# Performance work log

Measured on AMD Instinct MI355X. Metric: run time of the kernel, lower is better.

## Reference

```python
import jax, jax.numpy as jnp
import numpy as np

N_NODES = 100000
N_EDGES = 1600000
D_IN = 128
D_OUT = 128


def setup_inputs() -> dict:
    key = jax.random.key(0)
    k_x, k_r, k_c, k_v, k_w = jax.random.split(key, 5)
    X = jax.random.normal(k_x, (N_NODES, D_IN), dtype=jnp.float32)
    A_rows = jax.random.randint(k_r, (N_EDGES,), 0, N_NODES, dtype=jnp.int32)
    A_cols = jax.random.randint(k_c, (N_EDGES,), 0, N_NODES, dtype=jnp.int32)
    A_vals = jax.random.uniform(k_v, (N_EDGES,), dtype=jnp.float32)
    # Xavier-uniform linear weight [out, in], zero bias (matches reset_parameters)
    limit = float(np.sqrt(6.0 / (D_IN + D_OUT)))
    W = jax.random.uniform(k_w, (D_OUT, D_IN), dtype=jnp.float32, minval=-limit, maxval=limit)
    b = jnp.zeros((D_OUT,), dtype=jnp.float32)
    return {"X": X, "A_rows": A_rows, "A_cols": A_cols, "A_vals": A_vals, "W": W, "b": b}


def reference(X, A_rows, A_cols, A_vals, W, b):
    # h = A_sparse @ X  (COO SpMM: gather neighbor features, scale, scatter-add by row)
    msgs = A_vals[:, None] * X[A_cols]          # [E, D_IN]
    h = jax.ops.segment_sum(msgs, A_rows, num_segments=N_NODES)  # [N, D_IN]
    # dense linear projection
    return h @ W.T + b
```

## Files before the change

### kernel.cpp

```cpp
#include <hip/hip_runtime.h>

#define N_NODES_C 100000
#define N_EDGES_C 1600000
#define D_C 128
#define NBKT 1563
#define RPB 64
#define CAP 1536
#define CAP_H 768
#define PTILE 4096
#define NPB ((N_EDGES_C + PTILE - 1) / PTILE)
#define NGB ((N_NODES_C + 63) / 64)
#define WB_STRIDE 136

static __device__ __forceinline__ unsigned short f2bf(float x) {
    unsigned u = __float_as_uint(x);
    unsigned r = 0x7fffu + ((u >> 16) & 1u);
    return (unsigned short)((u + r) >> 16);
}
static __device__ __forceinline__ float bflo(unsigned u) { return __uint_as_float(u << 16); }
static __device__ __forceinline__ float bfhi(unsigned u) { return __uint_as_float(u & 0xffff0000u); }

typedef __attribute__((ext_vector_type(8))) __bf16 bf16x8;
typedef __attribute__((ext_vector_type(4))) float f32x4;
union FragU { uint4 u; bf16x8 b; };

__global__ __launch_bounds__(256) void prep(const float* __restrict__ W,
                                            unsigned short* __restrict__ Wbf,
                                            int* __restrict__ gcount) {
    int t = blockIdx.x * 256 + threadIdx.x;
    if (t < 4096) {
        float4 w = ((const float4*)W)[t];
        uint2 p;
        p.x = (unsigned)f2bf(w.x) | ((unsigned)f2bf(w.y) << 16);
        p.y = (unsigned)f2bf(w.z) | ((unsigned)f2bf(w.w) << 16);
        ((uint2*)Wbf)[t] = p;
    } else {
        int j = t - 4096;
        if (j < NBKT) gcount[j] = 0;
    }
}

union SMemF {
    struct {
        int lhist[NBKT];
        int lbase[NBKT];
        unsigned short ebkt[PTILE];
        unsigned short ernk[PTILE];
    } part;
    unsigned short ytile[4][16 * WB_STRIDE];
};

__global__ __launch_bounds__(256) void fused(const float* __restrict__ X,
                                             const int* __restrict__ rows,
                                             const int* __restrict__ cols,
                                             const float* __restrict__ vals,
                                             const unsigned short* __restrict__ Wbf,
                                             int* __restrict__ gcount,
                                             int2* __restrict__ staging,
                                             unsigned short* __restrict__ Y,
                                             int n, int E) {
    __shared__ SMemF sm;
    const int tid = threadIdx.x;

    if (blockIdx.x < NPB) {
        const int t0 = blockIdx.x * PTILE;

        for (int i = tid; i < NBKT; i += 256) sm.part.lhist[i] = 0;
        __syncthreads();

#pragma unroll
        for (int k = 0; k < PTILE / 256; ++k) {
            int e = t0 + k * 256 + tid;
            if (e < E) {
                int bkt = rows[e] >> 6;
                int rnk = atomicAdd(&sm.part.lhist[bkt], 1);
                sm.part.ebkt[k * 256 + tid] = (unsigned short)bkt;
                sm.part.ernk[k * 256 + tid] = (unsigned short)rnk;
            }
        }
        __syncthreads();

        for (int i = tid; i < NBKT; i += 256)
            sm.part.lbase[i] = sm.part.lhist[i] ? atomicAdd(&gcount[i], sm.part.lhist[i]) : 0;
        __syncthreads();

#pragma unroll
        for (int k = 0; k < PTILE / 256; ++k) {
            int e = t0 + k * 256 + tid;
            if (e < E) {
                int li = k * 256 + tid;
                int bkt = sm.part.ebkt[li];
                int dst = sm.part.lbase[bkt] + sm.part.ernk[li];
                if (dst < CAP) {
                    int rl = rows[e] & (RPB - 1);
                    int2 p;
                    p.x = cols[e] | (rl << 17);
                    p.y = __float_as_int(vals[e]);
                    staging[(long)bkt * CAP + dst] = p;
                }
            }
        }
        return;
    }

    const int g = blockIdx.x - NPB;
    const int wave = tid >> 6;
    const int lane = tid & 63;
    const int m16 = lane & 15;
    const int quad = lane >> 4;

    const int row0 = g * 64 + wave * 16;
    int row = row0 + m16;
    int rowc = (row < n) ? row : (n - 1);

    FragU a[4];
    const float* xp = X + (long)rowc * D_C + quad * 8;
#pragma unroll
    for (int s = 0; s < 4; ++s) {
        float4 x0 = *(const float4*)(xp + s * 32);
        float4 x1 = *(const float4*)(xp + s * 32 + 4);
        a[s].u.x = (unsigned)f2bf(x0.x) | ((unsigned)f2bf(x0.y) << 16);
        a[s].u.y = (unsigned)f2bf(x0.z) | ((unsigned)f2bf(x0.w) << 16);
        a[s].u.z = (unsigned)f2bf(x1.x) | ((unsigned)f2bf(x1.y) << 16);
        a[s].u.w = (unsigned)f2bf(x1.z) | ((unsigned)f2bf(x1.w) << 16);
    }

    f32x4 acc[8];
#pragma unroll
    for (int t = 0; t < 8; ++t) acc[t] = (f32x4){0.f, 0.f, 0.f, 0.f};

#pragma unroll
    for (int s = 0; s < 4; ++s) {
#pragma unroll
        for (int t = 0; t < 8; ++t) {
            FragU bf;
            bf.u = *(const uint4*)&Wbf[(t * 16 + m16) * D_C + s * 32 + quad * 8];
            acc[t] = __builtin_amdgcn_mfma_f32_16x16x32_bf16(a[s].b, bf.b, acc[t], 0, 0, 0);
        }
    }

    unsigned short* yt = sm.ytile[wave];
#pragma unroll
    for (int t = 0; t < 8; ++t)
#pragma unroll
        for (int r = 0; r < 4; ++r)
            yt[(quad * 4 + r) * WB_STRIDE + t * 16 + m16] = f2bf(acc[t][r]);
    __syncthreads();

#pragma unroll
    for (int h = 0; h < 2; ++h) {
        int row_l = h * 8 + (lane >> 3);
        int orow = row0 + row_l;
        if (orow < n) {
            const unsigned short* src = &yt[row_l * WB_STRIDE + (lane & 7) * 16];
            uint4 v0 = *(const uint4*)(src);
            uint4 v1 = *(const uint4*)(src + 8);
            uint4* dst = (uint4*)&Y[(long)orow * D_C + (lane & 7) * 16];
            dst[0] = v0;
            dst[1] = v1;
        }
    }
}

__global__ __launch_bounds__(256) void sort_aggregate(const int* __restrict__ gcount,
                                                      const int2* __restrict__ staging,
                                                      const unsigned short* __restrict__ Y,
                                                      const float* __restrict__ bias,
                                                      float* __restrict__ out, int n) {
    __shared__ int2 pl[CAP_H];
    __shared__ int hist[32];
    __shared__ int lcur[32];
    __shared__ int rbegL[32];
    __shared__ int rcntL[32];

    const int bb = blockIdx.x >> 1;
    const int half = blockIdx.x & 1;
    const int tid = threadIdx.x;
    int cnt = gcount[bb];
    if (cnt > CAP) cnt = CAP;
    const long s = (long)bb * CAP;

    if (tid < 32) hist[tid] = 0;
    __syncthreads();

    const unsigned* sx = (const unsigned*)(staging + s);
    for (int i = tid; i < cnt; i += 256) {
        int rl = sx[2 * i] >> 17;
        if ((rl >> 5) == half) atomicAdd(&hist[rl & 31], 1);
    }
    __syncthreads();

    int v = (tid < 32) ? hist[tid] : 0;
    for (int off = 1; off < 32; off <<= 1) {
        int t = (tid >= off && tid < 32) ? hist[tid - off] : 0;
        __syncthreads();
        if (tid < 32) hist[tid] += t;
        __syncthreads();
    }
    if (tid < 32) {
        int excl = hist[tid] - v;
        lcur[tid] = excl;
        rbegL[tid] = excl;
        rcntL[tid] = v;
    }
    __syncthreads();

    for (int i = tid; i < cnt; i += 256) {
        int2 p = staging[s + i];
        int rl = ((unsigned)p.x) >> 17;
        if ((rl >> 5) == half) {
            int slot = atomicAdd(&lcur[rl & 31], 1);
            if (slot < CAP_H) pl[slot] = p;
        }
    }
    __syncthreads();

    const int lane = tid & 15;
    const unsigned short* Yl = Y + lane * 8;
    float4 b0 = *(const float4*)&bias[lane * 8];
    float4 b1 = *(const float4*)&bias[lane * 8 + 4];

#pragma unroll
    for (int pass = 0; pass < 2; ++pass) {
        int rlocal = pass * 16 + (tid >> 4);
        int row = bb * RPB + half * 32 + rlocal;
        if (row >= n) continue;

        int i = rbegL[rlocal];
        int e = i + rcntL[rlocal];
        if (e > CAP_H) e = CAP_H;

        float acc[8];
        acc[0] = b0.x; acc[1] = b0.y; acc[2] = b0.z; acc[3] = b0.w;
        acc[4] = b1.x; acc[5] = b1.y; acc[6] = b1.z; acc[7] = b1.w;

        for (; i + 8 <= e; i += 8) {
            int2 p[8];
            uint4 y[8];
#pragma unroll
            for (int u = 0; u < 8; ++u) p[u] = pl[i + u];
#pragma unroll
            for (int u = 0; u < 8; ++u)
                y[u] = *(const uint4*)&Yl[(long)(p[u].x & 0x1FFFF) * D_C];
#pragma unroll
            for (int u = 0; u < 8; ++u) {
                float v2 = __int_as_float(p[u].y);
                acc[0] += v2 * bflo(y[u].x); acc[1] += v2 * bfhi(y[u].x);
                acc[2] += v2 * bflo(y[u].y); acc[3] += v2 * bfhi(y[u].y);
                acc[4] += v2 * bflo(y[u].z); acc[5] += v2 * bfhi(y[u].z);
                acc[6] += v2 * bflo(y[u].w); acc[7] += v2 * bfhi(y[u].w);
            }
        }
        for (; i + 4 <= e; i += 4) {
            int2 p[4];
            uint4 y[4];
#pragma unroll
            for (int u = 0; u < 4; ++u) p[u] = pl[i + u];
#pragma unroll
            for (int u = 0; u < 4; ++u)
                y[u] = *(const uint4*)&Yl[(long)(p[u].x & 0x1FFFF) * D_C];
#pragma unroll
            for (int u = 0; u < 4; ++u) {
                float v2 = __int_as_float(p[u].y);
                acc[0] += v2 * bflo(y[u].x); acc[1] += v2 * bfhi(y[u].x);
                acc[2] += v2 * bflo(y[u].y); acc[3] += v2 * bfhi(y[u].y);
                acc[4] += v2 * bflo(y[u].z); acc[5] += v2 * bfhi(y[u].z);
                acc[6] += v2 * bflo(y[u].w); acc[7] += v2 * bfhi(y[u].w);
            }
        }
        for (; i < e; ++i) {
            int2 p = pl[i];
            uint4 y = *(const uint4*)&Yl[(long)(p.x & 0x1FFFF) * D_C];
            float v2 = __int_as_float(p.y);
            acc[0] += v2 * bflo(y.x); acc[1] += v2 * bfhi(y.x);
            acc[2] += v2 * bflo(y.y); acc[3] += v2 * bfhi(y.y);
            acc[4] += v2 * bflo(y.z); acc[5] += v2 * bfhi(y.z);
            acc[6] += v2 * bflo(y.w); acc[7] += v2 * bfhi(y.w);
        }

        f32x4 o0 = {acc[0], acc[1], acc[2], acc[3]};
        f32x4 o1 = {acc[4], acc[5], acc[6], acc[7]};
        f32x4* op = (f32x4*)&out[(long)row * D_C + lane * 8];
        __builtin_nontemporal_store(o0, op);
        __builtin_nontemporal_store(o1, op + 1);
    }
}

__global__ __launch_bounds__(256) void gemm_mfma(const float* __restrict__ X,
                                                 const float* __restrict__ W,
                                                 unsigned short* __restrict__ Y, int n) {
    __shared__ unsigned short Wb[128 * WB_STRIDE];

    const int tid = threadIdx.x;
    const int wave = tid >> 6;
    const int lane = tid & 63;
    const int m16 = lane & 15;
    const int quad = lane >> 4;

    const int row0 = blockIdx.x * 64 + wave * 16;
    int row = row0 + m16;
    int rowc = (row < n) ? row : (n - 1);

    float4 xv[4][2];
    const float* xp = X + (long)rowc * D_C + quad * 8;
#pragma unroll
    for (int s = 0; s < 4; ++s) {
        xv[s][0] = *(const float4*)(xp + s * 32);
        xv[s][1] = *(const float4*)(xp + s * 32 + 4);
    }

    for (int i = tid; i < 128 * 32; i += 256) {
        int o = i >> 5;
        int k4 = (i & 31) * 4;
        float4 w = *(const float4*)&W[o * 128 + k4];
        uint2 p;
        p.x = (unsigned)f2bf(w.x) | ((unsigned)f2bf(w.y) << 16);
        p.y = (unsigned)f2bf(w.z) | ((unsigned)f2bf(w.w) << 16);
        *(uint2*)&Wb[o * WB_STRIDE + k4] = p;
    }
    __syncthreads();

    FragU a[4];
#pragma unroll
    for (int s = 0; s < 4; ++s) {
        a[s].u.x = (unsigned)f2bf(xv[s][0].x) | ((unsigned)f2bf(xv[s][0].y) << 16);
        a[s].u.y = (unsigned)f2bf(xv[s][0].z) | ((unsigned)f2bf(xv[s][0].w) << 16);
        a[s].u.z = (unsigned)f2bf(xv[s][1].x) | ((unsigned)f2bf(xv[s][1].y) << 16);
        a[s].u.w = (unsigned)f2bf(xv[s][1].z) | ((unsigned)f2bf(xv[s][1].w) << 16);
    }

    f32x4 acc[8];
#pragma unroll
    for (int t = 0; t < 8; ++t) acc[t] = (f32x4){0.f, 0.f, 0.f, 0.f};

#pragma unroll
    for (int s = 0; s < 4; ++s) {
#pragma unroll
        for (int t = 0; t < 8; ++t) {
            FragU bf;
            bf.u = *(const uint4*)&Wb[(t * 16 + m16) * WB_STRIDE + s * 32 + quad * 8];
            acc[t] = __builtin_amdgcn_mfma_f32_16x16x32_bf16(a[s].b, bf.b, acc[t], 0, 0, 0);
        }
    }

#pragma unroll
    for (int t = 0; t < 8; ++t) {
#pragma unroll
        for (int r = 0; r < 4; ++r) {
            int orow = row0 + quad * 4 + r;
            if (orow < n) Y[(long)orow * D_C + t * 16 + m16] = f2bf(acc[t][r]);
        }
    }
}

__global__ __launch_bounds__(256) void init_out(const float* __restrict__ b,
                                                float* __restrict__ out, int n) {
    int idx = blockIdx.x * 256 + threadIdx.x;
    int total = n * (D_C / 4);
    if (idx < total) {
        int o4 = idx & (D_C / 4 - 1);
        ((float4*)out)[idx] = ((const float4*)b)[o4];
    }
}

__global__ __launch_bounds__(256) void scatter_edges(const int* __restrict__ rows,
                                                     const int* __restrict__ cols,
                                                     const float* __restrict__ vals,
                                                     const unsigned short* __restrict__ Y,
                                                     float* __restrict__ out, int E) {
    int e = blockIdx.x * 8 + (threadIdx.x >> 5);
    if (e >= E) return;
    int lane = threadIdx.x & 31;
    int row = rows[e];
    int col = cols[e];
    float v = vals[e];
    uint2 y = *(const uint2*)&Y[(long)col * D_C + lane * 4];
    float* dst = out + (long)row * D_C + lane * 4;
    unsafeAtomicAdd(dst + 0, v * bflo(y.x));
    unsafeAtomicAdd(dst + 1, v * bfhi(y.x));
    unsafeAtomicAdd(dst + 2, v * bflo(y.y));
    unsafeAtomicAdd(dst + 3, v * bfhi(y.y));
}

extern "C" void kernel_launch(void* const* d_in, const int* in_sizes, int n_in,
                              void* d_out, int out_size, void* d_ws, size_t ws_size,
                              hipStream_t stream) {
    const float* X  = (const float*)d_in[0];
    const int*   Ar = (const int*)d_in[1];
    const int*   Ac = (const int*)d_in[2];
    const float* Av = (const float*)d_in[3];
    const float* W  = (const float*)d_in[4];
    const float* b  = (const float*)d_in[5];
    float* out = (float*)d_out;

    unsigned short* Y = (unsigned short*)d_ws;
    int2* staging = (int2*)(Y + 12800000);
    unsigned short* Wbf = (unsigned short*)(staging + (size_t)NBKT * CAP);
    int* gcount = (int*)(Wbf + 16384);
    size_t need = (size_t)12800000 * 2 + (size_t)NBKT * CAP * 8 + 32768 + (size_t)NBKT * 4;

    if (ws_size >= need) {
        prep<<<23, 256, 0, stream>>>(W, Wbf, gcount);
        fused<<<NPB + NGB, 256, 0, stream>>>(X, Ar, Ac, Av, Wbf, gcount, staging, Y,
                                             N_NODES_C, N_EDGES_C);
        sort_aggregate<<<2 * NBKT, 256, 0, stream>>>(gcount, staging, Y, b, out, N_NODES_C);
    } else {
        gemm_mfma<<<(N_NODES_C + 63) / 64, 256, 0, stream>>>(X, W, Y, N_NODES_C);
        init_out<<<(N_NODES_C * (D_C / 4) + 255) / 256, 256, 0, stream>>>(b, out, N_NODES_C);
        scatter_edges<<<(N_EDGES_C + 7) / 8, 256, 0, stream>>>(Ar, Ac, Av, Y, out, N_EDGES_C);
    }
}
```

Baseline: 242.0 us.

## Merge prep, partition/GEMM and aggregate into one cooperative persistent kernel

After: 412.4 us. 70.4% more time.

```diff
diff --git a/kernel.cpp b/kernel.cpp
--- a/kernel.cpp
+++ b/kernel.cpp
@@ -1,4 +1,7 @@
 #include <hip/hip_runtime.h>
+#include <hip/hip_cooperative_groups.h>
+
+namespace cg = cooperative_groups;
 
 #define N_NODES_C 100000
 #define N_EDGES_C 1600000
@@ -7,7 +10,7 @@
 #define RPB 64
 #define CAP 1536
 #define CAP_H 768
-#define PTILE 4096
+#define PTILE 2048
 #define NPB ((N_EDGES_C + PTILE - 1) / PTILE)
 #define NGB ((N_NODES_C + 63) / 64)
 #define WB_STRIDE 136
@@ -23,6 +26,292 @@
 typedef __attribute__((ext_vector_type(8))) __bf16 bf16x8;
 typedef __attribute__((ext_vector_type(4))) float f32x4;
 union FragU { uint4 u; bf16x8 b; };
+
+union SMemAll {
+    struct {
+        int lhist[NBKT];
+        int lbase[NBKT];
+        unsigned short ebkt[PTILE];
+        unsigned short ernk[PTILE];
+    } part;
+    unsigned short ytile[4][16 * WB_STRIDE];
+    struct {
+        int2 pl[CAP_H];
+        int hist[32];
+        int lcur[32];
+        int rb[32];
+        int rc[32];
+    } agg;
+};
+
+static __device__ __forceinline__ void partition_item(SMemAll& sm, int item,
+        const int* __restrict__ rows, const int* __restrict__ cols,
+        const float* __restrict__ vals, int* __restrict__ gcount,
+        int2* __restrict__ staging, int E) {
+    const int tid = threadIdx.x;
+    const int t0 = item * PTILE;
+
+    for (int i = tid; i < NBKT; i += 256) sm.part.lhist[i] = 0;
+    __syncthreads();
+
+#pragma unroll
+    for (int k = 0; k < PTILE / 256; ++k) {
+        int e = t0 + k * 256 + tid;
+        if (e < E) {
+            int bkt = rows[e] >> 6;
+            int rnk = atomicAdd(&sm.part.lhist[bkt], 1);
+            sm.part.ebkt[k * 256 + tid] = (unsigned short)bkt;
+            sm.part.ernk[k * 256 + tid] = (unsigned short)rnk;
+        }
+    }
+    __syncthreads();
+
+    for (int i = tid; i < NBKT; i += 256)
+        sm.part.lbase[i] = sm.part.lhist[i] ? atomicAdd(&gcount[i], sm.part.lhist[i]) : 0;
+    __syncthreads();
+
+#pragma unroll
+    for (int k = 0; k < PTILE / 256; ++k) {
+        int e = t0 + k * 256 + tid;
+        if (e < E) {
+            int li = k * 256 + tid;
+            int bkt = sm.part.ebkt[li];
+            int dst = sm.part.lbase[bkt] + sm.part.ernk[li];
+            if (dst < CAP) {
+                int rl = rows[e] & (RPB - 1);
+                int2 p;
+                p.x = cols[e] | (rl << 17);
+                p.y = __float_as_int(vals[e]);
+                staging[(long)bkt * CAP + dst] = p;
+            }
+        }
+    }
+}
+
+static __device__ __forceinline__ void gemm_item(SMemAll& sm, int g,
+        const float* __restrict__ X, const unsigned short* __restrict__ Wbf,
+        unsigned short* __restrict__ Y, int n) {
+    const int tid = threadIdx.x;
+    const int wave = tid >> 6;
+    const int lane = tid & 63;
+    const int m16 = lane & 15;
+    const int quad = lane >> 4;
+
+    const int row0 = g * 64 + wave * 16;
+    int row = row0 + m16;
+    int rowc = (row < n) ? row : (n - 1);
+
+    FragU a[4];
+    const float* xp = X + (long)rowc * D_C + quad * 8;
+#pragma unroll
+    for (int s = 0; s < 4; ++s) {
+        float4 x0 = *(const float4*)(xp + s * 32);
+        float4 x1 = *(const float4*)(xp + s * 32 + 4);
+        a[s].u.x = (unsigned)f2bf(x0.x) | ((unsigned)f2bf(x0.y) << 16);
+        a[s].u.y = (unsigned)f2bf(x0.z) | ((unsigned)f2bf(x0.w) << 16);
+        a[s].u.z = (unsigned)f2bf(x1.x) | ((unsigned)f2bf(x1.y) << 16);
+        a[s].u.w = (unsigned)f2bf(x1.z) | ((unsigned)f2bf(x1.w) << 16);
+    }
+
+    f32x4 acc[8];
+#pragma unroll
+    for (int t = 0; t < 8; ++t) acc[t] = (f32x4){0.f, 0.f, 0.f, 0.f};
+
+#pragma unroll
+    for (int s = 0; s < 4; ++s) {
+#pragma unroll
+        for (int t = 0; t < 8; ++t) {
+            FragU bf;
+            bf.u = *(const uint4*)&Wbf[(t * 16 + m16) * D_C + s * 32 + quad * 8];
+            acc[t] = __builtin_amdgcn_mfma_f32_16x16x32_bf16(a[s].b, bf.b, acc[t], 0, 0, 0);
+        }
+    }
+
+    unsigned short* yt = sm.ytile[wave];
+#pragma unroll
+    for (int t = 0; t < 8; ++t)
+#pragma unroll
+        for (int r = 0; r < 4; ++r)
+            yt[(quad * 4 + r) * WB_STRIDE + t * 16 + m16] = f2bf(acc[t][r]);
+    __syncthreads();
+
+#pragma unroll
+    for (int h = 0; h < 2; ++h) {
+        int row_l = h * 8 + (lane >> 3);
+        int orow = row0 + row_l;
+        if (orow < n) {
+            const unsigned short* src = &yt[row_l * WB_STRIDE + (lane & 7) * 16];
+            uint4 v0 = *(const uint4*)(src);
+            uint4 v1 = *(const uint4*)(src + 8);
+            uint4* dst = (uint4*)&Y[(long)orow * D_C + (lane & 7) * 16];
+            dst[0] = v0;
+            dst[1] = v1;
+        }
+    }
+}
+
+static __device__ __forceinline__ void agg_item(SMemAll& sm, int item,
+        const int* __restrict__ gcount, const int2* __restrict__ staging,
+        const unsigned short* __restrict__ Y, const float* __restrict__ bias,
+        float* __restrict__ out, int n) {
+    const int bb = item >> 1;
+    const int half = item & 1;
+    const int tid = threadIdx.x;
+    int cnt = gcount[bb];
+    if (cnt > CAP) cnt = CAP;
+    const long s = (long)bb * CAP;
+
+    if (tid < 32) sm.agg.hist[tid] = 0;
+    __syncthreads();
+
+    const unsigned* sx = (const unsigned*)(staging + s);
+    for (int i = tid; i < cnt; i += 256) {
+        int rl = sx[2 * i] >> 17;
+        if ((rl >> 5) == half) atomicAdd(&sm.agg.hist[rl & 31], 1);
+    }
+    __syncthreads();
+
+    int v = (tid < 32) ? sm.agg.hist[tid] : 0;
+    for (int off = 1; off < 32; off <<= 1) {
+        int t = (tid >= off && tid < 32) ? sm.agg.hist[tid - off] : 0;
+        __syncthreads();
+        if (tid < 32) sm.agg.hist[tid] += t;
+        __syncthreads();
+    }
+    if (tid < 32) {
+        int excl = sm.agg.hist[tid] - v;
+        sm.agg.lcur[tid] = excl;
+        sm.agg.rb[tid] = excl;
+        sm.agg.rc[tid] = v;
+    }
+    __syncthreads();
+
+    for (int i = tid; i < cnt; i += 256) {
+        int2 p = staging[s + i];
+        int rl = ((unsigned)p.x) >> 17;
+        if ((rl >> 5) == half) {
+            int slot = atomicAdd(&sm.agg.lcur[rl & 31], 1);
+            if (slot < CAP_H) sm.agg.pl[slot] = p;
+        }
+    }
+    __syncthreads();
+
+    const int lane = tid & 15;
+    const unsigned short* Yl = Y + lane * 8;
+    float4 b0 = *(const float4*)&bias[lane * 8];
+    float4 b1 = *(const float4*)&bias[lane * 8 + 4];
+
+#pragma unroll
+    for (int pass = 0; pass < 2; ++pass) {
+        int rlocal = pass * 16 + (tid >> 4);
+        int row = bb * RPB + half * 32 + rlocal;
+        if (row >= n) continue;
+
+        int i = sm.agg.rb[rlocal];
+        int e = i + sm.agg.rc[rlocal];
+        if (e > CAP_H) e = CAP_H;
+
+        float acc[8];
+        acc[0] = b0.x; acc[1] = b0.y; acc[2] = b0.z; acc[3] = b0.w;
+        acc[4] = b1.x; acc[5] = b1.y; acc[6] = b1.z; acc[7] = b1.w;
+
+        for (; i + 8 <= e; i += 8) {
+            int2 p[8];
+            uint4 y[8];
+#pragma unroll
+            for (int u = 0; u < 8; ++u) p[u] = sm.agg.pl[i + u];
+#pragma unroll
+            for (int u = 0; u < 8; ++u)
+                y[u] = *(const uint4*)&Yl[(long)(p[u].x & 0x1FFFF) * D_C];
+#pragma unroll
+            for (int u = 0; u < 8; ++u) {
+                float v2 = __int_as_float(p[u].y);
+                acc[0] += v2 * bflo(y[u].x); acc[1] += v2 * bfhi(y[u].x);
+                acc[2] += v2 * bflo(y[u].y); acc[3] += v2 * bfhi(y[u].y);
+                acc[4] += v2 * bflo(y[u].z); acc[5] += v2 * bfhi(y[u].z);
+                acc[6] += v2 * bflo(y[u].w); acc[7] += v2 * bfhi(y[u].w);
+            }
+        }
+        for (; i + 4 <= e; i += 4) {
+            int2 p[4];
+            uint4 y[4];
+#pragma unroll
+            for (int u = 0; u < 4; ++u) p[u] = sm.agg.pl[i + u];
+#pragma unroll
+            for (int u = 0; u < 4; ++u)
+                y[u] = *(const uint4*)&Yl[(long)(p[u].x & 0x1FFFF) * D_C];
+#pragma unroll
+            for (int u = 0; u < 4; ++u) {
+                float v2 = __int_as_float(p[u].y);
+                acc[0] += v2 * bflo(y[u].x); acc[1] += v2 * bfhi(y[u].x);
+                acc[2] += v2 * bflo(y[u].y); acc[3] += v2 * bfhi(y[u].y);
+                acc[4] += v2 * bflo(y[u].z); acc[5] += v2 * bfhi(y[u].z);
+                acc[6] += v2 * bflo(y[u].w); acc[7] += v2 * bfhi(y[u].w);
+            }
+        }
+        for (; i < e; ++i) {
+            int2 p = sm.agg.pl[i];
+            uint4 y = *(const uint4*)&Yl[(long)(p.x & 0x1FFFF) * D_C];
+            float v2 = __int_as_float(p.y);
+            acc[0] += v2 * bflo(y.x); acc[1] += v2 * bfhi(y.x);
+            acc[2] += v2 * bflo(y.y); acc[3] += v2 * bfhi(y.y);
+            acc[4] += v2 * bflo(y.z); acc[5] += v2 * bfhi(y.z);
+            acc[6] += v2 * bflo(y.w); acc[7] += v2 * bfhi(y.w);
+        }
+
+        f32x4 o0 = {acc[0], acc[1], acc[2], acc[3]};
+        f32x4 o1 = {acc[4], acc[5], acc[6], acc[7]};
+        f32x4* op = (f32x4*)&out[(long)row * D_C + lane * 8];
+        __builtin_nontemporal_store(o0, op);
+        __builtin_nontemporal_store(o1, op + 1);
+    }
+}
+
+__global__ __launch_bounds__(256) void fused_all(const float* __restrict__ X,
+                                                 const int* __restrict__ rows,
+                                                 const int* __restrict__ cols,
+                                                 const float* __restrict__ vals,
+                                                 const float* __restrict__ W,
+                                                 const float* __restrict__ bias,
+                                                 unsigned short* __restrict__ Wbf,
+                                                 int* __restrict__ gcount,
+                                                 int2* __restrict__ staging,
+                                                 unsigned short* __restrict__ Y,
+                                                 float* __restrict__ out,
+                                                 int n, int E) {
+    __shared__ SMemAll sm;
+    cg::grid_group grid = cg::this_grid();
+    const int nb = gridDim.x;
+
+    for (int t = blockIdx.x * 256 + threadIdx.x; t < 4096 + NBKT; t += nb * 256) {
+        if (t < 4096) {
+            float4 w = ((const float4*)W)[t];
+            uint2 p;
+            p.x = (unsigned)f2bf(w.x) | ((unsigned)f2bf(w.y) << 16);
+            p.y = (unsigned)f2bf(w.z) | ((unsigned)f2bf(w.w) << 16);
+            ((uint2*)Wbf)[t] = p;
+        } else {
+            gcount[t - 4096] = 0;
+        }
+    }
+    __threadfence();
+    grid.sync();
+
+    for (int item = blockIdx.x; item < NPB + NGB; item += nb) {
+        __syncthreads();
+        if (item < NPB)
+            partition_item(sm, item, rows, cols, vals, gcount, staging, E);
+        else
+            gemm_item(sm, item - NPB, X, Wbf, Y, n);
+    }
+    __threadfence();
+    grid.sync();
+
+    for (int item = blockIdx.x; item < 2 * NBKT; item += nb) {
+        __syncthreads();
+        agg_item(sm, item, gcount, staging, Y, bias, out, n);
+    }
+}
 
 __global__ __launch_bounds__(256) void prep(const float* __restrict__ W,
                                             unsigned short* __restrict__ Wbf,
@@ -40,16 +329,6 @@
     }
 }
 
-union SMemF {
-    struct {
-        int lhist[NBKT];
-        int lbase[NBKT];
-        unsigned short ebkt[PTILE];
-        unsigned short ernk[PTILE];
-    } part;
-    unsigned short ytile[4][16 * WB_STRIDE];
-};
-
 __global__ __launch_bounds__(256) void fused(const float* __restrict__ X,
                                              const int* __restrict__ rows,
                                              const int* __restrict__ cols,
@@ -59,107 +338,11 @@
                                              int2* __restrict__ staging,
                                              unsigned short* __restrict__ Y,
                                              int n, int E) {
-    __shared__ SMemF sm;
-    const int tid = threadIdx.x;
-
-    if (blockIdx.x < NPB) {
-        const int t0 = blockIdx.x * PTILE;
-
-        for (int i = tid; i < NBKT; i += 256) sm.part.lhist[i] = 0;
-        __syncthreads();
-
-#pragma unroll
-        for (int k = 0; k < PTILE / 256; ++k) {
-            int e = t0 + k * 256 + tid;
-            if (e < E) {
-                int bkt = rows[e] >> 6;
-                int rnk = atomicAdd(&sm.part.lhist[bkt], 1);
-                sm.part.ebkt[k * 256 + tid] = (unsigned short)bkt;
-                sm.part.ernk[k * 256 + tid] = (unsigned short)rnk;
-            }
-        }
-        __syncthreads();
-
-        for (int i = tid; i < NBKT; i += 256)
-            sm.part.lbase[i] = sm.part.lhist[i] ? atomicAdd(&gcount[i], sm.part.lhist[i]) : 0;
-        __syncthreads();
-
-#pragma unroll
-        for (int k = 0; k < PTILE / 256; ++k) {
-            int e = t0 + k * 256 + tid;
-            if (e < E) {
-                int li = k * 256 + tid;
-                int bkt = sm.part.ebkt[li];
-                int dst = sm.part.lbase[bkt] + sm.part.ernk[li];
-                if (dst < CAP) {
-                    int rl = rows[e] & (RPB - 1);
-                    int2 p;
-                    p.x = cols[e] | (rl << 17);
-                    p.y = __float_as_int(vals[e]);
-                    staging[(long)bkt * CAP + dst] = p;
-                }
-            }
-        }
-        return;
-    }
-
-    const int g = blockIdx.x - NPB;
-    const int wave = tid >> 6;
-    const int lane = tid & 63;
-    const int m16 = lane & 15;
-    const int quad = lane >> 4;
-
-    const int row0 = g * 64 + wave * 16;
-    int row = row0 + m16;
-    int rowc = (row < n) ? row : (n - 1);
-
-    FragU a[4];
-    const float* xp = X + (long)rowc * D_C + quad * 8;
-#pragma unroll
-    for (int s = 0; s < 4; ++s) {
-        float4 x0 = *(const float4*)(xp + s * 32);
-        float4 x1 = *(const float4*)(xp + s * 32 + 4);
-        a[s].u.x = (unsigned)f2bf(x0.x) | ((unsigned)f2bf(x0.y) << 16);
-        a[s].u.y = (unsigned)f2bf(x0.z) | ((unsigned)f2bf(x0.w) << 16);
-        a[s].u.z = (unsigned)f2bf(x1.x) | ((unsigned)f2bf(x1.y) << 16);
-        a[s].u.w = (unsigned)f2bf(x1.z) | ((unsigned)f2bf(x1.w) << 16);
-    }
-
-    f32x4 acc[8];
-#pragma unroll
-    for (int t = 0; t < 8; ++t) acc[t] = (f32x4){0.f, 0.f, 0.f, 0.f};
-
-#pragma unroll
-    for (int s = 0; s < 4; ++s) {
-#pragma unroll
-        for (int t = 0; t < 8; ++t) {
-            FragU bf;
-            bf.u = *(const uint4*)&Wbf[(t * 16 + m16) * D_C + s * 32 + quad * 8];
-            acc[t] = __builtin_amdgcn_mfma_f32_16x16x32_bf16(a[s].b, bf.b, acc[t], 0, 0, 0);
-        }
-    }
-
-    unsigned short* yt = sm.ytile[wave];
-#pragma unroll
-    for (int t = 0; t < 8; ++t)
-#pragma unroll
-        for (int r = 0; r < 4; ++r)
-            yt[(quad * 4 + r) * WB_STRIDE + t * 16 + m16] = f2bf(acc[t][r]);
-    __syncthreads();
-
-#pragma unroll
-    for (int h = 0; h < 2; ++h) {
-        int row_l = h * 8 + (lane >> 3);
-        int orow = row0 + row_l;
-        if (orow < n) {
-            const unsigned short* src = &yt[row_l * WB_STRIDE + (lane & 7) * 16];
-            uint4 v0 = *(const uint4*)(src);
-            uint4 v1 = *(const uint4*)(src + 8);
-            uint4* dst = (uint4*)&Y[(long)orow * D_C + (lane & 7) * 16];
-            dst[0] = v0;
-            dst[1] = v1;
-        }
-    }
+    __shared__ SMemAll sm;
+    if (blockIdx.x < NPB)
+        partition_item(sm, blockIdx.x, rows, cols, vals, gcount, staging, E);
+    else
+        gemm_item(sm, blockIdx.x - NPB, X, Wbf, Y, n);
 }
 
 __global__ __launch_bounds__(256) void sort_aggregate(const int* __restrict__ gcount,
@@ -167,123 +350,8 @@
                                                       const unsigned short* __restrict__ Y,
                                                       const float* __restrict__ bias,
                                                       float* __restrict__ out, int n) {
-    __shared__ int2 pl[CAP_H];
-    __shared__ int hist[32];
-    __shared__ int lcur[32];
-    __shared__ int rbegL[32];
-    __shared__ int rcntL[32];
-
-    const int bb = blockIdx.x >> 1;
-    const int half = blockIdx.x & 1;
-    const int tid = threadIdx.x;
-    int cnt = gcount[bb];
-    if (cnt > CAP) cnt = CAP;
-    const long s = (long)bb * CAP;
-
-    if (tid < 32) hist[tid] = 0;
-    __syncthreads();
-
-    const unsigned* sx = (const unsigned*)(staging + s);
-    for (int i = tid; i < cnt; i += 256) {
-        int rl = sx[2 * i] >> 17;
-        if ((rl >> 5) == half) atomicAdd(&hist[rl & 31], 1);
-    }
-    __syncthreads();
-
-    int v = (tid < 32) ? hist[tid] : 0;
-    for (int off = 1; off < 32; off <<= 1) {
-        int t = (tid >= off && tid < 32) ? hist[tid - off] : 0;
-        __syncthreads();
-        if (tid < 32) hist[tid] += t;
-        __syncthreads();
-    }
-    if (tid < 32) {
-        int excl = hist[tid] - v;
-        lcur[tid] = excl;
-        rbegL[tid] = excl;
-        rcntL[tid] = v;
-    }
-    __syncthreads();
-
-    for (int i = tid; i < cnt; i += 256) {
-        int2 p = staging[s + i];
-        int rl = ((unsigned)p.x) >> 17;
-        if ((rl >> 5) == half) {
-            int slot = atomicAdd(&lcur[rl & 31], 1);
-            if (slot < CAP_H) pl[slot] = p;
-        }
-    }
-    __syncthreads();
-
-    const int lane = tid & 15;
-    const unsigned short* Yl = Y + lane * 8;
-    float4 b0 = *(const float4*)&bias[lane * 8];
-    float4 b1 = *(const float4*)&bias[lane * 8 + 4];
-
-#pragma unroll
-    for (int pass = 0; pass < 2; ++pass) {
-        int rlocal = pass * 16 + (tid >> 4);
-        int row = bb * RPB + half * 32 + rlocal;
-        if (row >= n) continue;
-
-        int i = rbegL[rlocal];
-        int e = i + rcntL[rlocal];
-        if (e > CAP_H) e = CAP_H;
-
-        float acc[8];
-        acc[0] = b0.x; acc[1] = b0.y; acc[2] = b0.z; acc[3] = b0.w;
-        acc[4] = b1.x; acc[5] = b1.y; acc[6] = b1.z; acc[7] = b1.w;
-
-        for (; i + 8 <= e; i += 8) {
-            int2 p[8];
-            uint4 y[8];
-#pragma unroll
-            for (int u = 0; u < 8; ++u) p[u] = pl[i + u];
-#pragma unroll
-            for (int u = 0; u < 8; ++u)
-                y[u] = *(const uint4*)&Yl[(long)(p[u].x & 0x1FFFF) * D_C];
-#pragma unroll
-            for (int u = 0; u < 8; ++u) {
-                float v2 = __int_as_float(p[u].y);
-                acc[0] += v2 * bflo(y[u].x); acc[1] += v2 * bfhi(y[u].x);
-                acc[2] += v2 * bflo(y[u].y); acc[3] += v2 * bfhi(y[u].y);
-                acc[4] += v2 * bflo(y[u].z); acc[5] += v2 * bfhi(y[u].z);
-                acc[6] += v2 * bflo(y[u].w); acc[7] += v2 * bfhi(y[u].w);
-            }
-        }
-        for (; i + 4 <= e; i += 4) {
-            int2 p[4];
-            uint4 y[4];
-#pragma unroll
-            for (int u = 0; u < 4; ++u) p[u] = pl[i + u];
-#pragma unroll
-            for (int u = 0; u < 4; ++u)
-                y[u] = *(const uint4*)&Yl[(long)(p[u].x & 0x1FFFF) * D_C];
-#pragma unroll
-            for (int u = 0; u < 4; ++u) {
-                float v2 = __int_as_float(p[u].y);
-                acc[0] += v2 * bflo(y[u].x); acc[1] += v2 * bfhi(y[u].x);
-                acc[2] += v2 * bflo(y[u].y); acc[3] += v2 * bfhi(y[u].y);
-                acc[4] += v2 * bflo(y[u].z); acc[5] += v2 * bfhi(y[u].z);
-                acc[6] += v2 * bflo(y[u].w); acc[7] += v2 * bfhi(y[u].w);
-            }
-        }
-        for (; i < e; ++i) {
-            int2 p = pl[i];
-            uint4 y = *(const uint4*)&Yl[(long)(p.x & 0x1FFFF) * D_C];
-            float v2 = __int_as_float(p.y);
-            acc[0] += v2 * bflo(y.x); acc[1] += v2 * bfhi(y.x);
-            acc[2] += v2 * bflo(y.y); acc[3] += v2 * bfhi(y.y);
-            acc[4] += v2 * bflo(y.z); acc[5] += v2 * bfhi(y.z);
-            acc[6] += v2 * bflo(y.w); acc[7] += v2 * bfhi(y.w);
-        }
-
-        f32x4 o0 = {acc[0], acc[1], acc[2], acc[3]};
-        f32x4 o1 = {acc[4], acc[5], acc[6], acc[7]};
-        f32x4* op = (f32x4*)&out[(long)row * D_C + lane * 8];
-        __builtin_nontemporal_store(o0, op);
-        __builtin_nontemporal_store(o1, op + 1);
-    }
+    __shared__ SMemAll sm;
+    agg_item(sm, blockIdx.x, gcount, staging, Y, bias, out, n);
 }
 
 __global__ __launch_bounds__(256) void gemm_mfma(const float* __restrict__ X,
@@ -399,6 +467,35 @@
     int* gcount = (int*)(Wbf + 16384);
     size_t need = (size_t)12800000 * 2 + (size_t)NBKT * CAP * 8 + 32768 + (size_t)NBKT * 4;
 
+    static int coopGrid = -2;
+    if (coopGrid == -2) {
+        coopGrid = 0;
+        hipDeviceProp_t prop;
+        if (hipGetDeviceProperties(&prop, 0) == hipSuccess && prop.cooperativeLaunch) {
+            int maxB = 0;
+            if (hipOccupancyMaxActiveBlocksPerMultiprocessor(&maxB, fused_all, 256, 0)
+                    == hipSuccess && maxB > 0)
+                coopGrid = maxB * prop.multiProcessorCount;
+        }
+    }
+
+    if (ws_size >= need && coopGrid > 0) {
+        const float* X_ = X; const int* Ar_ = Ar; const int* Ac_ = Ac;
+        const float* Av_ = Av; const float* W_ = W; const float* b_ = b;
+        unsigned short* Wbf_ = Wbf; int* gcount_ = gcount; int2* staging_ = staging;
+        unsigned short* Y_ = Y; float* out_ = out;
+        int n_ = N_NODES_C, E_ = N_EDGES_C;
+        void* args[] = {(void*)&X_, (void*)&Ar_, (void*)&Ac_, (void*)&Av_,
+                        (void*)&W_, (void*)&b_, (void*)&Wbf_, (void*)&gcount_,
+                        (void*)&staging_, (void*)&Y_, (void*)&out_,
+                        (void*)&n_, (void*)&E_};
+        hipError_t err = hipLaunchCooperativeKernel((const void*)fused_all,
+                                                    dim3(coopGrid), dim3(256),
+                                                    args, 0, stream);
+        if (err == hipSuccess) return;
+        coopGrid = 0;
+    }
+
     if (ws_size >= need) {
         prep<<<23, 256, 0, stream>>>(W, Wbf, gcount);
         fused<<<NPB + NGB, 256, 0, stream>>>(X, Ar, Ac, Av, Wbf, gcount, staging, Y,
```
